# Kernel optimization log

Hardware: AMD Instinct MI355X
Metric: run time of the kernel (lower is better)

The kernel has to match this reference:

```python
import jax, jax.numpy as jnp
import numpy as np

ROUTING_ITERS = 3

def squash(t, axis=-1):
    norm = jnp.linalg.norm(t, axis=axis, keepdims=True)
    scale = norm ** 2 / (1 + norm ** 2)
    return scale * t / (norm + 1e-08)

def setup_inputs() -> dict:
    key = jax.random.key(0)
    k1, k2 = jax.random.split(key)
    B, R, C, Din, Dout = 64, 4608, 32, 16, 16
    x = jax.random.normal(k1, (B, R, Din), dtype=jnp.float32)
    route_weights = jax.random.normal(k2, (R, C, Din, Dout), dtype=jnp.float32)
    return {"x": x, "route_weights": route_weights}

def reference(x, route_weights):
    # x: [B, R, Din], route_weights: [R, C, Din, Dout]
    B, R, _ = x.shape
    C = route_weights.shape[1]
    # u_hat: [B, R, C, Dout]  (prediction vectors)
    u_hat = jnp.einsum('bri,rcio->brco', x, route_weights)
    b_ij = jnp.zeros((B, R, C, 1), dtype=u_hat.dtype)
    v_j = None
    for _ in range(ROUTING_ITERS):
        c_ij = jax.nn.softmax(b_ij, axis=2)                    # coupling coeffs over capsules
        s_j = jnp.sum(c_ij * u_hat, axis=1, keepdims=True)     # [B, 1, C, Dout]
        v_j = squash(s_j, axis=-1)                             # [B, 1, C, Dout]
        b_ij = b_ij + jnp.sum(u_hat * v_j, axis=-1, keepdims=True)
    return v_j[:, 0]                                           # [B, C, Dout]
```

## Files before the change

### kernel.cpp

```cpp
#include <hip/hip_runtime.h>
#include <math.h>


#define B_    64
#define R_    4608
#define C_    32
#define RB    36
#define NBLK  (R_ / RB)
#define SELEM 32768
#define CRPB  8
#define CWBLK (R_ / CRPB)

typedef _Float16 half8  __attribute__((ext_vector_type(8)));
typedef _Float16 half2v __attribute__((ext_vector_type(2)));
typedef float    f32x16 __attribute__((ext_vector_type(16)));

__device__ __forceinline__ void gload_lds16(const void* g, void* l) {
    __builtin_amdgcn_global_load_lds(
        (const __attribute__((address_space(1))) void*)g,
        (__attribute__((address_space(3))) void*)l, 16, 0, 0);
}

__global__ __launch_bounds__(512)
void caps_conv(const float* __restrict__ W, const float* __restrict__ x,
               _Float16* __restrict__ wp, _Float16* __restrict__ xa)
{
    const int tid = threadIdx.x;
    if (blockIdx.x >= CWBLK) {
        const int idx = (blockIdx.x - CWBLK) * 512 + tid;
        const int r = idx >> 6, b = idx & 63;
        const float4* xs = (const float4*)(x + ((size_t)b * R_ + r) * 16);
        const float4 A = xs[0], Bv = xs[1], Cv = xs[2], Dv = xs[3];
        half8 lo, hi;
        lo[0]=(_Float16)A.x;  lo[1]=(_Float16)A.y;  lo[2]=(_Float16)A.z;  lo[3]=(_Float16)A.w;
        lo[4]=(_Float16)Bv.x; lo[5]=(_Float16)Bv.y; lo[6]=(_Float16)Bv.z; lo[7]=(_Float16)Bv.w;
        hi[0]=(_Float16)Cv.x; hi[1]=(_Float16)Cv.y; hi[2]=(_Float16)Cv.z; hi[3]=(_Float16)Cv.w;
        hi[4]=(_Float16)Dv.x; hi[5]=(_Float16)Dv.y; hi[6]=(_Float16)Dv.z; hi[7]=(_Float16)Dv.w;
        half8* dst = (half8*)(xa + ((size_t)idx << 4));
        dst[0] = lo; dst[1] = hi;
        return;
    }

    __shared__ float wl[2][8192];
    const int r0    = blockIdx.x * CRPB;
    const int lane  = tid & 63;
    const int wavei = tid >> 6;
    const int h     = lane >> 5;
    const int l31   = lane & 31;
    const int o     = l31 & 15;
    const int cp    = l31 >> 4;

#define WSTAGE(buf, r)                                                          \
    do {                                                                        \
        const char* wsrc_ = (const char*)W + ((size_t)(r) << 15);               \
        _Pragma("unroll")                                                       \
        for (int j_ = 0; j_ < 4; ++j_) {                                        \
            const int D_ = (j_ << 13) + (tid << 4);                             \
            const int S_ = D_ ^ (((D_ >> 10) & 1) << 6);                        \
            gload_lds16(wsrc_ + S_, (char*)wl[buf] + D_);                       \
        }                                                                       \
    } while (0)

    WSTAGE(0, r0);

#pragma unroll 1
    for (int t = 0; t < CRPB; ++t) {
        __builtin_amdgcn_s_barrier();
        if (t + 1 < CRPB) {
            WSTAGE((t + 1) & 1, r0 + t + 1);
            asm volatile("s_waitcnt vmcnt(4)" ::: "memory");
        } else {
            asm volatile("s_waitcnt vmcnt(0)" ::: "memory");
        }
        __builtin_amdgcn_s_barrier();

        const char* lb = (const char*)wl[t & 1];
#pragma unroll
        for (int ci = 0; ci < 2; ++ci) {
            const int nt = ci * 8 + wavei;
            const int c  = 2 * nt + cp;
            const int base = c * 1024 + h * 512 + o * 4;
            const int key  = (c & 1) << 6;
            half8 f;
#pragma unroll
            for (int e = 0; e < 8; ++e)
                f[e] = (_Float16)*(const float*)(lb + ((base + e * 64) ^ key));
            *(half8*)(wp + (((size_t)(r0 + t) * 16 + nt) * 64 + lane) * 8) = f;
        }
    }
#undef WSTAGE
}

template<bool FIRST>
__global__ __launch_bounds__(1024, 4)
void caps_mfma(const _Float16* __restrict__ xa, const _Float16* __restrict__ wp,
               const float* __restrict__ vsumT, float* __restrict__ sdst)
{
    __shared__ _Float16 xalds[RB * 512];
    __shared__ float t_lds[32][33];
    __shared__ float c_lds[32][33];

    const int tid  = threadIdx.x;
    const int lane = tid & 63;
    const int wv   = tid >> 6;
    const int h    = lane >> 5;
    const int l31  = lane & 31;
    const int bh   = blockIdx.y;
    const int r0   = blockIdx.x * RB;
    const int bg   = bh * 32 + l31;

    {
        const int slx = (lane << 4) ^ (((lane >> 3) & 7) << 4);
        for (int t = wv; t < RB; t += 16) {
            const char* src = (const char*)xa + (size_t)(r0 + t) * 2048 + bh * 1024 + slx;
            gload_lds16(src, (char*)xalds + t * 1024);
        }
    }

    f32x16 sacc, zf;
#pragma unroll
    for (int k = 0; k < 16; ++k) { sacc[k] = 0.f; zf[k] = 0.f; }

    half2v vh[8];
    if (!FIRST) {
#pragma unroll
        for (int e = 0; e < 16; ++e) {
            const int g = wv * 32 + (e & 3) + 8 * (e >> 2) + 4 * h;
            vh[e >> 1][e & 1] = (_Float16)vsumT[(size_t)g * 64 + bg];
        }
    }

    asm volatile("s_waitcnt vmcnt(0)" ::: "memory");
    __syncthreads();

    const int avoff = ((l31 << 5) + (h << 4)) ^ (((l31 >> 2) & 7) << 4);

    const size_t wstride = 16 * 64 * 8;
    const _Float16* wpb = wp + (((size_t)r0 * 16 + wv) * 64 + lane) * 8;
    half8 bc = *(const half8*)wpb;

#pragma unroll 1
    for (int t = 0; t < RB; ++t) {
        const half8 av = *(const half8*)((const char*)xalds + t * 1024 + avoff);

        f32x16 u;
        if (FIRST) {
            sacc = __builtin_amdgcn_mfma_f32_32x32x16_f16(bc, av, sacc, 0, 0, 0);
        } else {
            u = __builtin_amdgcn_mfma_f32_32x32x16_f16(bc, av, zf, 0, 0, 0);
        }

        const int tn = (t < RB - 1) ? (t + 1) : t;
        bc = *(const half8*)(wp + ((size_t)(r0 + tn)) * wstride
                                + ((size_t)wv * 64 + lane) * 8);

        if (FIRST) continue;

        {
            float s0 = 0.f, s1 = 0.f;
#pragma unroll
            for (int e2 = 0; e2 < 4; ++e2) {
                s0 += u[2 * e2]         * (float)vh[e2][0];
                s0 += u[2 * e2 + 1]     * (float)vh[e2][1];
                s1 += u[8 + 2 * e2]     * (float)vh[4 + e2][0];
                s1 += u[8 + 2 * e2 + 1] * (float)vh[4 + e2][1];
            }
            s0 += __shfl_xor(s0, 32);
            s1 += __shfl_xor(s1, 32);
            if (h == 0) {
                t_lds[2 * wv    ][l31] = s0;
                t_lds[2 * wv + 1][l31] = s1;
            }
        }
        __syncthreads();

        if (tid < 512) {
            const int a_ = lane & 15;
            const int b2 = tid >> 4;
            const float tA = t_lds[2 * a_][b2];
            const float tB = t_lds[2 * a_ + 1][b2];
            float m = fmaxf(tA, tB);
            m = fmaxf(m, __shfl_xor(m, 1));
            m = fmaxf(m, __shfl_xor(m, 2));
            m = fmaxf(m, __shfl_xor(m, 4));
            m = fmaxf(m, __shfl_xor(m, 8));
            const float eA = __expf(tA - m);
            const float eB = __expf(tB - m);
            float zs = eA + eB;
            zs += __shfl_xor(zs, 1);
            zs += __shfl_xor(zs, 2);
            zs += __shfl_xor(zs, 4);
            zs += __shfl_xor(zs, 8);
            const float inv = 1.0f / zs;
            c_lds[2 * a_][b2]     = eA * inv;
            c_lds[2 * a_ + 1][b2] = eB * inv;
        }
        __syncthreads();

        {
            const float c0v = c_lds[2 * wv    ][l31];
            const float c1v = c_lds[2 * wv + 1][l31];
#pragma unroll
            for (int e = 0; e < 8; ++e)  sacc[e] += c0v * u[e];
#pragma unroll
            for (int e = 8; e < 16; ++e) sacc[e] += c1v * u[e];
        }
    }

    const float scale = FIRST ? 0.03125f : 1.0f;
    float* sp = sdst + ((size_t)blockIdx.x << 15);
#pragma unroll
    for (int e = 0; e < 16; ++e) {
        const int g = wv * 32 + (e & 3) + 8 * (e >> 2) + 4 * h;
        sp[(size_t)g * 64 + bg] = sacc[e] * scale;
    }
}

__global__ __launch_bounds__(256)
void caps_reduce1(const float* __restrict__ sp, float* __restrict__ s2)
{
    const int e  = blockIdx.x * 256 + threadIdx.x;
    const int pg = blockIdx.y;
    const float* p0 = sp + (size_t)pg * 16 * SELEM + e;
    float a = 0.0f;
#pragma unroll 8
    for (int p = 0; p < 16; ++p) a += p0[(size_t)p * SELEM];
    s2[pg * SELEM + e] = a;
}

__global__ __launch_bounds__(64)
void caps_reduce2T(const float* __restrict__ src, float* __restrict__ vsumT,
                   float* __restrict__ out, int mode)
{
    const int c = blockIdx.x;
    const int b = threadIdx.x;
    float a[16];
#pragma unroll
    for (int o = 0; o < 16; ++o) a[o] = 0.0f;
    for (int p = 0; p < 8; ++p)
#pragma unroll
        for (int o = 0; o < 16; ++o)
            a[o] += src[(size_t)p * SELEM + c * 1024 + o * 64 + b];
    float sq = 0.0f;
#pragma unroll
    for (int o = 0; o < 16; ++o) sq += a[o] * a[o];
    const float n  = sqrtf(sq);
    const float sc = sq / (1.0f + sq) / (n + 1e-8f);
    if (mode == 2) {
#pragma unroll
        for (int o = 0; o < 16; ++o)
            out[(size_t)b * 512 + c * 16 + o] = a[o] * sc;
    } else if (mode == 0) {
#pragma unroll
        for (int o = 0; o < 16; ++o)
            vsumT[c * 1024 + o * 64 + b] = a[o] * sc;
    } else {
#pragma unroll
        for (int o = 0; o < 16; ++o)
            vsumT[c * 1024 + o * 64 + b] += a[o] * sc;
    }
}

__global__ __launch_bounds__(256)
void caps_reduce2(const float* __restrict__ src, int P,
                  float* __restrict__ vsum, float* __restrict__ out, int mode)
{
    const int e = blockIdx.x * 256 + threadIdx.x;
    float a = 0.0f;
    for (int p = 0; p < P; ++p) a += src[(size_t)p * SELEM + e];
    float sq = a * a;
#pragma unroll
    for (int off = 8; off >= 1; off >>= 1) sq += __shfl_xor(sq, off);
    const float n = sqrtf(sq);
    const float v = a * (sq / (1.0f + sq) / (n + 1e-8f));
    if (mode == 0)      vsum[e] = v;
    else if (mode == 1) vsum[e] += v;
    else                out[e] = v;
}

template<bool FIRST>
__global__ __launch_bounds__(1024, 4)
void caps_pass_f32(const float* __restrict__ x, const float* __restrict__ W,
                   const float* __restrict__ vsumg, float* __restrict__ sdst)
{
    __shared__ float wlds[2][8192];
    const int tid = threadIdx.x, lane = tid & 63;
    const int c = tid & 31, dh = (tid >> 5) & 1, w = tid >> 6;
    const int r0 = blockIdx.x * RB, b0 = w << 2;
    const int key = (c & 7) << 4;
    const int cb  = (c << 10) + (dh << 5);

    float sacc[4][8];
#pragma unroll
    for (int q = 0; q < 4; ++q)
#pragma unroll
        for (int k = 0; k < 8; ++k) sacc[q][k] = 0.0f;

    float vreg[4][8];
    if (!FIRST) {
#pragma unroll
        for (int q = 0; q < 4; ++q) {
            const float4* vp = (const float4*)(vsumg + ((((b0+q) << 5) + c) << 4) + (dh << 3));
            float4 a = vp[0], bq = vp[1];
            vreg[q][0]=a.x; vreg[q][1]=a.y; vreg[q][2]=a.z; vreg[q][3]=a.w;
            vreg[q][4]=bq.x; vreg[q][5]=bq.y; vreg[q][6]=bq.z; vreg[q][7]=bq.w;
        }
    }

    const int Dloc0 = (w << 11);
    const int lx0 = (lane << 4) ^ ((((w << 1))     & 7) << 4);
    const int lx1 = (lane << 4) ^ ((((w << 1) | 1) & 7) << 4);
    const int wu = __builtin_amdgcn_readfirstlane(w);
    const float* xw = x + (size_t)((wu << 2) * R_ + r0) * 16;

#define STAGE(buf, r)                                                              \
    do {                                                                           \
        const char* wr_ = (const char*)W + ((size_t)(r) << 15);                    \
        gload_lds16(wr_ + Dloc0        + lx0, (char*)wlds[buf] + Dloc0);           \
        gload_lds16(wr_ + Dloc0 + 1024 + lx1, (char*)wlds[buf] + Dloc0 + 1024);    \
    } while (0)

    STAGE(0, r0);
#pragma unroll 1
    for (int t = 0; t < RB; ++t) {
        const int cur = t & 1;
        if (t + 1 < RB) { STAGE(cur ^ 1, r0 + t + 1); asm volatile("s_waitcnt vmcnt(2)" ::: "memory"); }
        else            { asm volatile("s_waitcnt vmcnt(0)" ::: "memory"); }
        __builtin_amdgcn_s_barrier();
        __builtin_amdgcn_sched_barrier(0);

        const char* lb = (const char*)wlds[cur];
        float u[4][8];
#pragma unroll
        for (int q = 0; q < 4; ++q)
#pragma unroll
            for (int k = 0; k < 8; ++k) u[q][k] = 0.0f;

#pragma unroll
        for (int i = 0; i < 16; ++i) {
            const int A = (cb + (i << 6)) ^ key;
            float4 w0 = *(const float4*)(lb + A);
            float4 w1 = *(const float4*)(lb + (A ^ 16));
            float wv[8] = {w0.x, w0.y, w0.z, w0.w, w1.x, w1.y, w1.z, w1.w};
#pragma unroll
            for (int q = 0; q < 4; ++q) {
                const float xv = xw[(size_t)q * (R_ * 16) + t * 16 + i];
#pragma unroll
                for (int k = 0; k < 8; ++k) u[q][k] = fmaf(xv, wv[k], u[q][k]);
            }
        }

#pragma unroll
        for (int q = 0; q < 4; ++q) {
            float cij;
            if (FIRST) cij = 0.03125f;
            else {
                float th = 0.0f;
#pragma unroll
                for (int k = 0; k < 8; ++k) th = fmaf(u[q][k], vreg[q][k], th);
                th += __shfl_xor(th, 32);
                float m = th;
#pragma unroll
                for (int off = 16; off >= 1; off >>= 1) m = fmaxf(m, __shfl_xor(m, off));
                const float e = __expf(th - m);
                float ssum = e;
#pragma unroll
                for (int off = 16; off >= 1; off >>= 1) ssum += __shfl_xor(ssum, off);
                cij = e / ssum;
            }
#pragma unroll
            for (int k = 0; k < 8; ++k) sacc[q][k] = fmaf(cij, u[q][k], sacc[q][k]);
        }
        __builtin_amdgcn_s_barrier();
    }
#undef STAGE

#pragma unroll
    for (int q = 0; q < 4; ++q) {
        float* sp = sdst + ((((b0+q) << 5) + c) << 4) + (dh << 3);
#pragma unroll
        for (int k = 0; k < 8; ++k) atomicAdd(sp + k, sacc[q][k]);
    }
}

extern "C" void kernel_launch(void* const* d_in, const int* in_sizes, int n_in,
                              void* d_out, int out_size, void* d_ws, size_t ws_size,
                              hipStream_t stream)
{
    const float* x = (const float*)d_in[0];
    const float* W = (const float*)d_in[1];
    float* out = (float*)d_out;

    const size_t WPB = (size_t)R_ * 16 * 64 * 8 * sizeof(_Float16);
    const size_t XAB = (size_t)R_ * 64 * 16 * sizeof(_Float16);
    const size_t SPB = (size_t)NBLK * SELEM * sizeof(float);
    const size_t S2B = (size_t)8 * SELEM * sizeof(float);
    const size_t VSB = (size_t)SELEM * sizeof(float);
    char* wsc = (char*)d_ws;
    const dim3 pgrid(NBLK, 2);

    if (ws_size >= WPB + XAB + SPB + S2B + VSB) {
        _Float16* wp  = (_Float16*)wsc;
        _Float16* xa  = (_Float16*)(wsc + WPB);
        float* s_part = (float*)(wsc + WPB + XAB);
        float* s2     = (float*)(wsc + WPB + XAB + SPB);
        float* vsumT  = (float*)(wsc + WPB + XAB + SPB + S2B);

        caps_conv<<<CWBLK + 576, 512, 0, stream>>>(W, x, wp, xa);

        caps_mfma<true ><<<pgrid, 1024, 0, stream>>>(xa, wp, nullptr, s_part);
        caps_reduce1<<<dim3(128, 8), 256, 0, stream>>>(s_part, s2);
        caps_reduce2T<<<32, 64, 0, stream>>>(s2, vsumT, nullptr, 0);

        caps_mfma<false><<<pgrid, 1024, 0, stream>>>(xa, wp, vsumT, s_part);
        caps_reduce1<<<dim3(128, 8), 256, 0, stream>>>(s_part, s2);
        caps_reduce2T<<<32, 64, 0, stream>>>(s2, vsumT, nullptr, 1);

        caps_mfma<false><<<pgrid, 1024, 0, stream>>>(xa, wp, vsumT, s_part);
        caps_reduce1<<<dim3(128, 8), 256, 0, stream>>>(s_part, s2);
        caps_reduce2T<<<32, 64, 0, stream>>>(s2, vsumT, out, 2);
    } else {
        float* s    = (float*)wsc;
        float* vsum = s + SELEM;

        hipMemsetAsync(s, 0, VSB, stream);
        caps_pass_f32<true><<<NBLK, 1024, 0, stream>>>(x, W, nullptr, s);
        caps_reduce2<<<128, 256, 0, stream>>>(s, 1, vsum, nullptr, 0);

        hipMemsetAsync(s, 0, VSB, stream);
        caps_pass_f32<false><<<NBLK, 1024, 0, stream>>>(x, W, vsum, s);
        caps_reduce2<<<128, 256, 0, stream>>>(s, 1, vsum, nullptr, 1);

        hipMemsetAsync(s, 0, VSB, stream);
        caps_pass_f32<false><<<NBLK, 1024, 0, stream>>>(x, W, vsum, s);
        caps_reduce2<<<128, 256, 0, stream>>>(s, 1, nullptr, out, 2);
    }
}
```

Measured before the change: 163.0 us.

## Fuse weight fp16 conversion into MFMA routing passes via LDS staging

Drops the separate pre-pass that converted route weights to a packed fp16 layout. Each routing pass now streams the fp32 weights straight into double-buffered LDS with async global-to-LDS loads and converts them to fp16 in registers before the MFMA. This removes one full read of the fp32 weights plus the write of the packed copy. In exchange each of the three passes reads fp32 weights, twice the bytes of the fp16 copy, and adds LDS traffic and per-step barriers inside the routing loop.

```diff
diff --git a/kernel.cpp b/kernel.cpp
--- a/kernel.cpp
+++ b/kernel.cpp
@@ -8,8 +8,6 @@
 #define RB    36
 #define NBLK  (R_ / RB)
 #define SELEM 32768
-#define CRPB  8
-#define CWBLK (R_ / CRPB)
 
 typedef _Float16 half8  __attribute__((ext_vector_type(8)));
 typedef _Float16 half2v __attribute__((ext_vector_type(2)));
@@ -22,80 +20,27 @@
 }
 
 __global__ __launch_bounds__(512)
-void caps_conv(const float* __restrict__ W, const float* __restrict__ x,
-               _Float16* __restrict__ wp, _Float16* __restrict__ xa)
-{
-    const int tid = threadIdx.x;
-    if (blockIdx.x >= CWBLK) {
-        const int idx = (blockIdx.x - CWBLK) * 512 + tid;
-        const int r = idx >> 6, b = idx & 63;
-        const float4* xs = (const float4*)(x + ((size_t)b * R_ + r) * 16);
-        const float4 A = xs[0], Bv = xs[1], Cv = xs[2], Dv = xs[3];
-        half8 lo, hi;
-        lo[0]=(_Float16)A.x;  lo[1]=(_Float16)A.y;  lo[2]=(_Float16)A.z;  lo[3]=(_Float16)A.w;
-        lo[4]=(_Float16)Bv.x; lo[5]=(_Float16)Bv.y; lo[6]=(_Float16)Bv.z; lo[7]=(_Float16)Bv.w;
-        hi[0]=(_Float16)Cv.x; hi[1]=(_Float16)Cv.y; hi[2]=(_Float16)Cv.z; hi[3]=(_Float16)Cv.w;
-        hi[4]=(_Float16)Dv.x; hi[5]=(_Float16)Dv.y; hi[6]=(_Float16)Dv.z; hi[7]=(_Float16)Dv.w;
-        half8* dst = (half8*)(xa + ((size_t)idx << 4));
-        dst[0] = lo; dst[1] = hi;
-        return;
-    }
-
-    __shared__ float wl[2][8192];
-    const int r0    = blockIdx.x * CRPB;
-    const int lane  = tid & 63;
-    const int wavei = tid >> 6;
-    const int h     = lane >> 5;
-    const int l31   = lane & 31;
-    const int o     = l31 & 15;
-    const int cp    = l31 >> 4;
-
-#define WSTAGE(buf, r)                                                          \
-    do {                                                                        \
-        const char* wsrc_ = (const char*)W + ((size_t)(r) << 15);               \
-        _Pragma("unroll")                                                       \
-        for (int j_ = 0; j_ < 4; ++j_) {                                        \
-            const int D_ = (j_ << 13) + (tid << 4);                             \
-            const int S_ = D_ ^ (((D_ >> 10) & 1) << 6);                        \
-            gload_lds16(wsrc_ + S_, (char*)wl[buf] + D_);                       \
-        }                                                                       \
-    } while (0)
-
-    WSTAGE(0, r0);
-
-#pragma unroll 1
-    for (int t = 0; t < CRPB; ++t) {
-        __builtin_amdgcn_s_barrier();
-        if (t + 1 < CRPB) {
-            WSTAGE((t + 1) & 1, r0 + t + 1);
-            asm volatile("s_waitcnt vmcnt(4)" ::: "memory");
-        } else {
-            asm volatile("s_waitcnt vmcnt(0)" ::: "memory");
-        }
-        __builtin_amdgcn_s_barrier();
-
-        const char* lb = (const char*)wl[t & 1];
-#pragma unroll
-        for (int ci = 0; ci < 2; ++ci) {
-            const int nt = ci * 8 + wavei;
-            const int c  = 2 * nt + cp;
-            const int base = c * 1024 + h * 512 + o * 4;
-            const int key  = (c & 1) << 6;
-            half8 f;
-#pragma unroll
-            for (int e = 0; e < 8; ++e)
-                f[e] = (_Float16)*(const float*)(lb + ((base + e * 64) ^ key));
-            *(half8*)(wp + (((size_t)(r0 + t) * 16 + nt) * 64 + lane) * 8) = f;
-        }
-    }
-#undef WSTAGE
+void caps_xconv(const float* __restrict__ x, _Float16* __restrict__ xa)
+{
+    const int idx = blockIdx.x * 512 + threadIdx.x;
+    const int r = idx >> 6, b = idx & 63;
+    const float4* xs = (const float4*)(x + ((size_t)b * R_ + r) * 16);
+    const float4 A = xs[0], Bv = xs[1], Cv = xs[2], Dv = xs[3];
+    half8 lo, hi;
+    lo[0]=(_Float16)A.x;  lo[1]=(_Float16)A.y;  lo[2]=(_Float16)A.z;  lo[3]=(_Float16)A.w;
+    lo[4]=(_Float16)Bv.x; lo[5]=(_Float16)Bv.y; lo[6]=(_Float16)Bv.z; lo[7]=(_Float16)Bv.w;
+    hi[0]=(_Float16)Cv.x; hi[1]=(_Float16)Cv.y; hi[2]=(_Float16)Cv.z; hi[3]=(_Float16)Cv.w;
+    hi[4]=(_Float16)Dv.x; hi[5]=(_Float16)Dv.y; hi[6]=(_Float16)Dv.z; hi[7]=(_Float16)Dv.w;
+    half8* dst = (half8*)(xa + ((size_t)idx << 4));
+    dst[0] = lo; dst[1] = hi;
 }
 
 template<bool FIRST>
 __global__ __launch_bounds__(1024, 4)
-void caps_mfma(const _Float16* __restrict__ xa, const _Float16* __restrict__ wp,
+void caps_mfma(const _Float16* __restrict__ xa, const float* __restrict__ Wg,
                const float* __restrict__ vsumT, float* __restrict__ sdst)
 {
+    __shared__ float wl[2][8192];
     __shared__ _Float16 xalds[RB * 512];
     __shared__ float t_lds[32][33];
     __shared__ float c_lds[32][33];
@@ -117,6 +62,19 @@
         }
     }
 
+#define WSTAGE(buf, r)                                                          \
+    do {                                                                        \
+        const char* wsrc_ = (const char*)Wg + ((size_t)(r) << 15);              \
+        _Pragma("unroll")                                                       \
+        for (int j_ = 0; j_ < 2; ++j_) {                                        \
+            const int D_ = (j_ << 14) + (tid << 4);                             \
+            const int S_ = D_ ^ (((D_ >> 10) & 1) << 6);                        \
+            gload_lds16(wsrc_ + S_, (char*)wl[buf] + D_);                       \
+        }                                                                       \
+    } while (0)
+
+    WSTAGE(0, r0);
+
     f32x16 sacc, zf;
 #pragma unroll
     for (int k = 0; k < 16; ++k) { sacc[k] = 0.f; zf[k] = 0.f; }
@@ -134,27 +92,37 @@
     __syncthreads();
 
     const int avoff = ((l31 << 5) + (h << 4)) ^ (((l31 >> 2) & 7) << 4);
-
-    const size_t wstride = 16 * 64 * 8;
-    const _Float16* wpb = wp + (((size_t)r0 * 16 + wv) * 64 + lane) * 8;
-    half8 bc = *(const half8*)wpb;
+    const int c_    = 2 * wv + (l31 >> 4);
+    const int wbase = c_ * 1024 + h * 512 + (l31 & 15) * 4;
+    const int wkey  = (c_ & 1) << 6;
 
 #pragma unroll 1
     for (int t = 0; t < RB; ++t) {
+        const int cur = t & 1;
+
+        if (FIRST) __builtin_amdgcn_s_barrier();
+        if (t + 1 < RB) {
+            WSTAGE(cur ^ 1, r0 + t + 1);
+            asm volatile("s_waitcnt vmcnt(2)" ::: "memory");
+        } else {
+            asm volatile("s_waitcnt vmcnt(0)" ::: "memory");
+        }
+        __builtin_amdgcn_s_barrier();
+
+        const char* lb = (const char*)wl[cur];
+        half8 bc;
+#pragma unroll
+        for (int e = 0; e < 8; ++e)
+            bc[e] = (_Float16)*(const float*)(lb + ((wbase + (e << 6)) ^ wkey));
+
         const half8 av = *(const half8*)((const char*)xalds + t * 1024 + avoff);
 
         f32x16 u;
         if (FIRST) {
             sacc = __builtin_amdgcn_mfma_f32_32x32x16_f16(bc, av, sacc, 0, 0, 0);
-        } else {
-            u = __builtin_amdgcn_mfma_f32_32x32x16_f16(bc, av, zf, 0, 0, 0);
-        }
-
-        const int tn = (t < RB - 1) ? (t + 1) : t;
-        bc = *(const half8*)(wp + ((size_t)(r0 + tn)) * wstride
-                                + ((size_t)wv * 64 + lane) * 8);
-
-        if (FIRST) continue;
+            continue;
+        }
+        u = __builtin_amdgcn_mfma_f32_32x32x16_f16(bc, av, zf, 0, 0, 0);
 
         {
             float s0 = 0.f, s1 = 0.f;
@@ -206,6 +174,7 @@
             for (int e = 8; e < 16; ++e) sacc[e] += c1v * u[e];
         }
     }
+#undef WSTAGE
 
     const float scale = FIRST ? 0.03125f : 1.0f;
     float* sp = sdst + ((size_t)blockIdx.x << 15);
@@ -391,7 +360,6 @@
     const float* W = (const float*)d_in[1];
     float* out = (float*)d_out;
 
-    const size_t WPB = (size_t)R_ * 16 * 64 * 8 * sizeof(_Float16);
     const size_t XAB = (size_t)R_ * 64 * 16 * sizeof(_Float16);
     const size_t SPB = (size_t)NBLK * SELEM * sizeof(float);
     const size_t S2B = (size_t)8 * SELEM * sizeof(float);
@@ -399,24 +367,23 @@
     char* wsc = (char*)d_ws;
     const dim3 pgrid(NBLK, 2);
 
-    if (ws_size >= WPB + XAB + SPB + S2B + VSB) {
-        _Float16* wp  = (_Float16*)wsc;
-        _Float16* xa  = (_Float16*)(wsc + WPB);
-        float* s_part = (float*)(wsc + WPB + XAB);
-        float* s2     = (float*)(wsc + WPB + XAB + SPB);
-        float* vsumT  = (float*)(wsc + WPB + XAB + SPB + S2B);
-
-        caps_conv<<<CWBLK + 576, 512, 0, stream>>>(W, x, wp, xa);
-
-        caps_mfma<true ><<<pgrid, 1024, 0, stream>>>(xa, wp, nullptr, s_part);
+    if (ws_size >= XAB + SPB + S2B + VSB) {
+        _Float16* xa  = (_Float16*)wsc;
+        float* s_part = (float*)(wsc + XAB);
+        float* s2     = (float*)(wsc + XAB + SPB);
+        float* vsumT  = (float*)(wsc + XAB + SPB + S2B);
+
+        caps_xconv<<<576, 512, 0, stream>>>(x, xa);
+
+        caps_mfma<true ><<<pgrid, 1024, 0, stream>>>(xa, W, nullptr, s_part);
         caps_reduce1<<<dim3(128, 8), 256, 0, stream>>>(s_part, s2);
         caps_reduce2T<<<32, 64, 0, stream>>>(s2, vsumT, nullptr, 0);
 
-        caps_mfma<false><<<pgrid, 1024, 0, stream>>>(xa, wp, vsumT, s_part);
+        caps_mfma<false><<<pgrid, 1024, 0, stream>>>(xa, W, vsumT, s_part);
         caps_reduce1<<<dim3(128, 8), 256, 0, stream>>>(s_part, s2);
         caps_reduce2T<<<32, 64, 0, stream>>>(s2, vsumT, nullptr, 1);
 
-        caps_mfma<false><<<pgrid, 1024, 0, stream>>>(xa, wp, vsumT, s_part);
+        caps_mfma<false><<<pgrid, 1024, 0, stream>>>(xa, W, vsumT, s_part);
         caps_reduce1<<<dim3(128, 8), 256, 0, stream>>>(s_part, s2);
         caps_reduce2T<<<32, 64, 0, stream>>>(s2, vsumT, out, 2);
     } else {
```

Result: slower. 181.7 us (+11.5%).
